# Performance work log

Hardware: AMD Instinct MI355X
Metric: run time of the kernel (lower is better)

The kernel has to match this reference:

```python
import jax, jax.numpy as jnp
import numpy as np

B = 32      # batch
N = 1024    # input_size (= maxval)
EPS = 1.0   # regularization_strength


def _isotonic_l2(y):
    """Non-increasing isotonic regression (L2) of each row of y: [B, n].

    Uses the minimax characterization  sol_i = min_{j<=i} max_{k>=i} mean(y[j..k]),
    which equals the PAV solution and yields the correct block-averaging Jacobian
    under autodiff. O(n^2) memory per row, fully vectorized.
    """
    b, n = y.shape
    cs = jnp.concatenate([jnp.zeros((b, 1), y.dtype), jnp.cumsum(y, axis=-1)], axis=-1)  # [B, n+1]
    j = jnp.arange(n)[:, None]   # start index
    k = jnp.arange(n)[None, :]   # end index
    length = (k - j + 1).astype(y.dtype)
    # M[b, j, k] = mean(y[b, j..k]) for k >= j
    M = (cs[:, None, 1:] - cs[:, :-1, None]) / jnp.where(k >= j, length, jnp.ones_like(length))
    M = jnp.where(k >= j, M, -jnp.inf)
    # Amax[b, j, i] = max_{k >= i} M[b, j, k]  (suffix max along k)
    Amax = jax.lax.cummax(M, axis=2, reverse=True)
    # restrict to j <= i, then minimize over j
    Amax = jnp.where(j <= k, Amax, jnp.inf)  # here the k-axis plays the role of i
    return jnp.min(Amax, axis=1)  # [B, n]


def _soft_rank(x, eps):
    """fast-soft-sort soft_rank, direction=ASCENDING, regularization='l2'."""
    b, n = x.shape
    theta = x / eps
    perm = jnp.argsort(-theta, axis=-1)                 # descending sort permutation
    s = jnp.take_along_axis(theta, perm, axis=-1)       # sorted (descending)
    w = jnp.arange(n, 0, -1, dtype=x.dtype)             # [n, n-1, ..., 1]
    sol = _isotonic_l2(s - w)                           # dual solution
    primal = s - sol                                    # projection, sorted order
    inv = jnp.argsort(perm, axis=-1)
    return jnp.take_along_axis(primal, inv, axis=-1)    # unpermute -> ranks in [1, n]


def setup_inputs() -> dict:
    key = jax.random.key(0)
    x = jax.random.normal(key, (B, N), dtype=jnp.float32)
    return {"x": x}


def reference(x) -> jnp.ndarray:
    ranks = _soft_rank(x, EPS)                          # [B, n]
    n = x.shape[1]
    t = jnp.arange(1, n + 1, dtype=x.dtype)             # rank targets 1..n
    # out[b, j, i] = relu(1 - |ranks[b, j] - (i + 1)|)  (== torch .permute(0, 2, 1) result)
    return jax.nn.relu(1.0 - jnp.abs(ranks[:, :, None] - t[None, None, :]))
```

## Files before the change

### kernel.cpp

```cpp
#include <hip/hip_runtime.h>
#include <stdint.h>

#define N 1024
#define BATCH 32

typedef float nfloat4 __attribute__((ext_vector_type(4)));

__global__ __launch_bounds__(256) void ranks_kernel(const float* __restrict__ x,
                                                    float* __restrict__ ranks) {
    __shared__ uint64_t keys[N];
    __shared__ float    ss[N];
    __shared__ float    yv[N];
    __shared__ double   csum[N];
    __shared__ int      segid[N];
    __shared__ int      run_start[N+1];
    __shared__ float    run_mean[N];
    __shared__ int      stk_cnt[N];
    __shared__ int      stk_runs[N];
    __shared__ double   wsumD[4];
    __shared__ int      wsumI[4];

    const int b = blockIdx.x;
    const int t = threadIdx.x;
    const int j0 = t << 2;
    const int lane = t & 63;
    const int wid = t >> 6;

    const float4 xq = reinterpret_cast<const float4*>(x + b * N)[t];
    {
        const float vv[4] = {xq.x, xq.y, xq.z, xq.w};
        #pragma unroll
        for (int e = 0; e < 4; ++e) {
            uint32_t u = __float_as_uint(vv[e]);
            u ^= (u & 0x80000000u) ? 0xFFFFFFFFu : 0x80000000u;
            keys[j0 + e] = (((uint64_t)u) << 10) | (uint64_t)(1023 - (j0 + e));
        }
    }
    __syncthreads();

    const uint64_t k0 = keys[j0 + 0];
    const uint64_t k1 = keys[j0 + 1];
    const uint64_t k2 = keys[j0 + 2];
    const uint64_t k3 = keys[j0 + 3];
    int c0 = 0, c1 = 0, c2 = 0, c3 = 0;
    for (int k = 0; k < N; k += 2) {
        const uint64_t ka = keys[k];
        const uint64_t kb = keys[k + 1];
        c0 += (ka > k0); c1 += (ka > k1); c2 += (ka > k2); c3 += (ka > k3);
        c0 += (kb > k0); c1 += (kb > k1); c2 += (kb > k2); c3 += (kb > k3);
    }
    ss[c0] = xq.x; ss[c1] = xq.y; ss[c2] = xq.z; ss[c3] = xq.w;
    __syncthreads();

    float4 yq;
    {
        const float4 sq = reinterpret_cast<const float4*>(ss)[t];
        yq.x = sq.x + (float)(j0 - 512);
        yq.y = sq.y + (float)(j0 - 511);
        yq.z = sq.z + (float)(j0 - 510);
        yq.w = sq.w + (float)(j0 - 509);
        reinterpret_cast<float4*>(yv)[t] = yq;
    }
    __syncthreads();

    const float ye[4] = {yq.x, yq.y, yq.z, yq.w};
    int    fl[4];
    int    lf[4];
    double lys[4];
    {
        float prev = (j0 == 0) ? -1.0e30f : yv[j0 - 1];
        double accy = 0.0; int accf = 0;
        #pragma unroll
        for (int e = 0; e < 4; ++e) {
            const int f = (prev > ye[e]) ? 1 : 0;
            prev = ye[e];
            fl[e] = f;
            accf += f;           lf[e]  = accf;
            accy += (double)ye[e]; lys[e] = accy;
        }
    }
    double vy = lys[3]; int vf = lf[3];
    #pragma unroll
    for (int off = 1; off < 64; off <<= 1) {
        const double oy = __shfl_up(vy, off);
        const int    of = __shfl_up(vf, off);
        if (lane >= off) { vy += oy; vf += of; }
    }
    if (lane == 63) { wsumD[wid] = vy; wsumI[wid] = vf; }
    __syncthreads();
    {
        double basey = vy - lys[3]; int basef = vf - lf[3];
        for (int w = 0; w < wid; ++w) { basey += wsumD[w]; basef += wsumI[w]; }
        #pragma unroll
        for (int e = 0; e < 4; ++e) {
            const int p   = j0 + e;
            const int seg = basef + lf[e];
            segid[p] = seg;
            csum[p]  = basey + lys[e];
            if (fl[e]) run_start[seg] = p;
        }
        if (t == 0) run_start[0] = 0;
    }
    __syncthreads();

    if (t == 0) {
        const int R = segid[N - 1] + 1;
        run_start[R] = N;
        double* stk_sum = reinterpret_cast<double*>(keys);
        int sp = 0;
        for (int r = 0; r < R; ++r) {
            const int a   = run_start[r];
            const int bnd = run_start[r + 1];
            double s = csum[bnd - 1] - ((a > 0) ? csum[a - 1] : 0.0);
            int    c = bnd - a;
            int    nr = 1;
            while (sp > 0 && s * (double)stk_cnt[sp - 1] > stk_sum[sp - 1] * (double)c) {
                s  += stk_sum[sp - 1];
                c  += stk_cnt[sp - 1];
                nr += stk_runs[sp - 1];
                --sp;
            }
            stk_sum[sp] = s; stk_cnt[sp] = c; stk_runs[sp] = nr; ++sp;
        }
        int rc = 0;
        for (int e2 = 0; e2 < sp; ++e2) {
            const float m = (float)(stk_sum[e2] / (double)stk_cnt[e2]);
            for (int q = 0; q < stk_runs[e2]; ++q) run_mean[rc++] = m;
        }
    }
    __syncthreads();

    float4 r4;
    r4.x = xq.x - run_mean[segid[c0]] + 512.0f;
    r4.y = xq.y - run_mean[segid[c1]] + 512.0f;
    r4.z = xq.z - run_mean[segid[c2]] + 512.0f;
    r4.w = xq.w - run_mean[segid[c3]] + 512.0f;
    reinterpret_cast<float4*>(ranks + b * N)[t] = r4;
}

__global__ __launch_bounds__(256) void fill_kernel(const float* __restrict__ ranks,
                                                   float* __restrict__ out) {
    const int row = blockIdx.x;
    const float r = ranks[row];
    const int i = threadIdx.x << 2;
    nfloat4 o;
    o.x = fmaxf(1.0f - fabsf(r - (float)(i + 1)), 0.0f);
    o.y = fmaxf(1.0f - fabsf(r - (float)(i + 2)), 0.0f);
    o.z = fmaxf(1.0f - fabsf(r - (float)(i + 3)), 0.0f);
    o.w = fmaxf(1.0f - fabsf(r - (float)(i + 4)), 0.0f);
    __builtin_nontemporal_store(o, reinterpret_cast<nfloat4*>(out + (size_t)row * N) + threadIdx.x);
}

extern "C" void kernel_launch(void* const* d_in, const int* in_sizes, int n_in,
                              void* d_out, int out_size, void* d_ws, size_t ws_size,
                              hipStream_t stream) {
    const float* x = (const float*)d_in[0];
    float* out = (float*)d_out;
    float* ranks = (float*)d_ws;

    ranks_kernel<<<BATCH, 256, 0, stream>>>(x, ranks);
    fill_kernel<<<BATCH * N, 256, 0, stream>>>(ranks, out);
}
```

Baseline: 163.4 us.

## Split rank counting into a separate parallel kernel and widen fill rows per block

Moves the O(n^2) rank-by-counting sort out of the 32-block ranks kernel into a new count kernel with 256 blocks. Each block handles 128 elements of one row, with its comparisons split across two thread halves, which spreads the work over far more CUs. The ranks kernel now reads the precomputed positions from workspace. Separately, the fill kernel writes four output rows per block, cutting the block count by four. This adds one more launch and a global round trip for the positions.

```diff
diff --git a/kernel.cpp b/kernel.cpp
--- a/kernel.cpp
+++ b/kernel.cpp
@@ -6,15 +6,55 @@
 
 typedef float nfloat4 __attribute__((ext_vector_type(4)));
 
+__global__ __launch_bounds__(256) void count_kernel(const float* __restrict__ x,
+                                                    int* __restrict__ pos_g) {
+    __shared__ uint64_t keys[N];
+    __shared__ int      partial[256];
+
+    const int row   = blockIdx.x >> 3;
+    const int chunk = blockIdx.x & 7;
+    const int t     = threadIdx.x;
+
+    const float4 xq = reinterpret_cast<const float4*>(x + row * N)[t];
+    {
+        const float vv[4] = {xq.x, xq.y, xq.z, xq.w};
+        const int j0 = t << 2;
+        #pragma unroll
+        for (int e = 0; e < 4; ++e) {
+            uint32_t u = __float_as_uint(vv[e]);
+            u ^= (u & 0x80000000u) ? 0xFFFFFFFFu : 0x80000000u;
+            keys[j0 + e] = (((uint64_t)u) << 10) | (uint64_t)(1023 - (j0 + e));
+        }
+    }
+    __syncthreads();
+
+    const int e    = (chunk << 7) + (t & 127);
+    const int half = t >> 7;
+    const uint64_t kk = keys[e];
+    const int kbeg = half << 9;
+    int c = 0;
+    for (int k = kbeg; k < kbeg + 512; k += 4) {
+        c += (int)(keys[k    ] > kk);
+        c += (int)(keys[k + 1] > kk);
+        c += (int)(keys[k + 2] > kk);
+        c += (int)(keys[k + 3] > kk);
+    }
+    partial[t] = c;
+    __syncthreads();
+
+    if (t < 128) pos_g[row * N + e] = partial[t] + partial[t + 128];
+}
+
 __global__ __launch_bounds__(256) void ranks_kernel(const float* __restrict__ x,
+                                                    const int* __restrict__ pos_g,
                                                     float* __restrict__ ranks) {
-    __shared__ uint64_t keys[N];
     __shared__ float    ss[N];
     __shared__ float    yv[N];
     __shared__ double   csum[N];
     __shared__ int      segid[N];
     __shared__ int      run_start[N+1];
     __shared__ float    run_mean[N];
+    __shared__ double   stk_sum[N];
     __shared__ int      stk_cnt[N];
     __shared__ int      stk_runs[N];
     __shared__ double   wsumD[4];
@@ -27,29 +67,8 @@
     const int wid = t >> 6;
 
     const float4 xq = reinterpret_cast<const float4*>(x + b * N)[t];
-    {
-        const float vv[4] = {xq.x, xq.y, xq.z, xq.w};
-        #pragma unroll
-        for (int e = 0; e < 4; ++e) {
-            uint32_t u = __float_as_uint(vv[e]);
-            u ^= (u & 0x80000000u) ? 0xFFFFFFFFu : 0x80000000u;
-            keys[j0 + e] = (((uint64_t)u) << 10) | (uint64_t)(1023 - (j0 + e));
-        }
-    }
-    __syncthreads();
-
-    const uint64_t k0 = keys[j0 + 0];
-    const uint64_t k1 = keys[j0 + 1];
-    const uint64_t k2 = keys[j0 + 2];
-    const uint64_t k3 = keys[j0 + 3];
-    int c0 = 0, c1 = 0, c2 = 0, c3 = 0;
-    for (int k = 0; k < N; k += 2) {
-        const uint64_t ka = keys[k];
-        const uint64_t kb = keys[k + 1];
-        c0 += (ka > k0); c1 += (ka > k1); c2 += (ka > k2); c3 += (ka > k3);
-        c0 += (kb > k0); c1 += (kb > k1); c2 += (kb > k2); c3 += (kb > k3);
-    }
-    ss[c0] = xq.x; ss[c1] = xq.y; ss[c2] = xq.z; ss[c3] = xq.w;
+    const int4   pq = reinterpret_cast<const int4*>(pos_g + b * N)[t];
+    ss[pq.x] = xq.x; ss[pq.y] = xq.y; ss[pq.z] = xq.z; ss[pq.w] = xq.w;
     __syncthreads();
 
     float4 yq;
@@ -75,7 +94,7 @@
             const int f = (prev > ye[e]) ? 1 : 0;
             prev = ye[e];
             fl[e] = f;
-            accf += f;           lf[e]  = accf;
+            accf += f;             lf[e]  = accf;
             accy += (double)ye[e]; lys[e] = accy;
         }
     }
@@ -106,7 +125,6 @@
     if (t == 0) {
         const int R = segid[N - 1] + 1;
         run_start[R] = N;
-        double* stk_sum = reinterpret_cast<double*>(keys);
         int sp = 0;
         for (int r = 0; r < R; ++r) {
             const int a   = run_start[r];
@@ -131,24 +149,33 @@
     __syncthreads();
 
     float4 r4;
-    r4.x = xq.x - run_mean[segid[c0]] + 512.0f;
-    r4.y = xq.y - run_mean[segid[c1]] + 512.0f;
-    r4.z = xq.z - run_mean[segid[c2]] + 512.0f;
-    r4.w = xq.w - run_mean[segid[c3]] + 512.0f;
+    r4.x = xq.x - run_mean[segid[pq.x]] + 512.0f;
+    r4.y = xq.y - run_mean[segid[pq.y]] + 512.0f;
+    r4.z = xq.z - run_mean[segid[pq.z]] + 512.0f;
+    r4.w = xq.w - run_mean[segid[pq.w]] + 512.0f;
     reinterpret_cast<float4*>(ranks + b * N)[t] = r4;
 }
 
 __global__ __launch_bounds__(256) void fill_kernel(const float* __restrict__ ranks,
                                                    float* __restrict__ out) {
-    const int row = blockIdx.x;
-    const float r = ranks[row];
+    const int r0 = blockIdx.x << 2;
     const int i = threadIdx.x << 2;
-    nfloat4 o;
-    o.x = fmaxf(1.0f - fabsf(r - (float)(i + 1)), 0.0f);
-    o.y = fmaxf(1.0f - fabsf(r - (float)(i + 2)), 0.0f);
-    o.z = fmaxf(1.0f - fabsf(r - (float)(i + 3)), 0.0f);
-    o.w = fmaxf(1.0f - fabsf(r - (float)(i + 4)), 0.0f);
-    __builtin_nontemporal_store(o, reinterpret_cast<nfloat4*>(out + (size_t)row * N) + threadIdx.x);
+    const float ra = ranks[r0 + 0];
+    const float rb = ranks[r0 + 1];
+    const float rc = ranks[r0 + 2];
+    const float rd = ranks[r0 + 3];
+    const float rv[4] = {ra, rb, rc, rd};
+    #pragma unroll
+    for (int rr = 0; rr < 4; ++rr) {
+        const float r = rv[rr];
+        nfloat4 o;
+        o.x = fmaxf(1.0f - fabsf(r - (float)(i + 1)), 0.0f);
+        o.y = fmaxf(1.0f - fabsf(r - (float)(i + 2)), 0.0f);
+        o.z = fmaxf(1.0f - fabsf(r - (float)(i + 3)), 0.0f);
+        o.w = fmaxf(1.0f - fabsf(r - (float)(i + 4)), 0.0f);
+        __builtin_nontemporal_store(o,
+            reinterpret_cast<nfloat4*>(out + (size_t)(r0 + rr) * N) + threadIdx.x);
+    }
 }
 
 extern "C" void kernel_launch(void* const* d_in, const int* in_sizes, int n_in,
@@ -156,8 +183,10 @@
                               hipStream_t stream) {
     const float* x = (const float*)d_in[0];
     float* out = (float*)d_out;
-    float* ranks = (float*)d_ws;
+    int*   pos_g = (int*)d_ws;
+    float* ranks = (float*)d_ws + BATCH * N;
 
-    ranks_kernel<<<BATCH, 256, 0, stream>>>(x, ranks);
-    fill_kernel<<<BATCH * N, 256, 0, stream>>>(ranks, out);
+    count_kernel<<<BATCH * 8, 256, 0, stream>>>(x, pos_g);
+    ranks_kernel<<<BATCH, 256, 0, stream>>>(x, pos_g, ranks);
+    fill_kernel<<<(BATCH * N) / 4, 256, 0, stream>>>(ranks, out);
 }
```

Measured after the change: 147.8 us. 9.6% less time.
